# Kernel tuning notes

Hardware: AMD Instinct MI355X
Metric: run time of the kernel (lower is better)

Reference implementation:

```python
import jax, jax.numpy as jnp
import numpy as np

B, C, T = 32, 273, 4096
CHOUT = 270
N_SUBJECTS = 200
POS_DIM = 256
MARGIN = 0.2
INVALID = -0.1
N_FREQS = int((POS_DIM // 2) ** 0.5)          # 11
ACTUAL_POS_DIM = N_FREQS * N_FREQS * 2        # 242
NEG_INF = -1e9  # exp(-1e9)==0 in fp32, identical softmax to -inf but grad-safe


def fourier_emb(positions):
    # positions: [..., 2] -> [..., 2*n_freqs^2]
    freqs = jnp.arange(N_FREQS, dtype=positions.dtype)
    width = 1.0 + 2.0 * MARGIN
    p = positions + MARGIN
    scale = 2.0 * np.pi / width
    # loc[..., i, j] = x * f_i * scale + y * f_j * scale
    loc = (p[..., 0, None, None] * (scale * freqs[:, None])
           + p[..., 1, None, None] * (scale * freqs[None, :]))
    loc = loc.reshape(*positions.shape[:-1], N_FREQS * N_FREQS)
    return jnp.concatenate([jnp.cos(loc), jnp.sin(loc)], axis=-1)


def setup_inputs() -> dict:
    key = jax.random.key(0)
    k1, k2, k3, k4 = jax.random.split(key, 4)
    meg = jax.random.normal(k1, (B, C, T), dtype=jnp.float32)
    positions = jax.random.uniform(k2, (B, C, 2), dtype=jnp.float32)
    # last 16 channels per sample are invalid (sentinel -0.1 on both coords)
    positions = positions.at[:, -16:, :].set(INVALID)
    subject_index = jax.random.randint(k3, (B,), 0, N_SUBJECTS)
    heads = jax.random.normal(k4, (N_SUBJECTS, CHOUT, ACTUAL_POS_DIM),
                              dtype=jnp.float32) / np.sqrt(ACTUAL_POS_DIM)
    return {"meg": meg, "positions": positions,
            "subject_index": subject_index, "heads": heads}


def reference(meg, positions, subject_index, heads):
    # meg: [B,C,T], positions: [B,C,2], subject_index: [B],
    # heads: [n_subjects, chout, pos_dim]
    embedding = fourier_emb(positions)                       # [B,C,D]
    invalid = jnp.all(positions == INVALID, axis=-1)         # [B,C]
    score_offset = jnp.where(invalid, NEG_INF, 0.0).astype(meg.dtype)
    h = heads[subject_index]                                 # [B,chout,D] per-subject gather
    scores = jnp.einsum('bcd,bod->boc', embedding, h) + score_offset[:, None, :]
    weights = jax.nn.softmax(scores, axis=2)                 # softmax over channels
    out = jnp.einsum('bct,boc->bot', meg, weights)           # [B,chout,T]
    return out
```

## Files before the change

kernel.cpp:

```cpp
#include <hip/hip_runtime.h>

#define NB 32
#define NC 273
#define NT 4096
#define NO 270
#define ND 242
#define CK 288
#define TSUB 128
#define NSUB 4

typedef __attribute__((ext_vector_type(8))) short short8;
typedef __attribute__((ext_vector_type(4))) float f32x4;

__device__ __forceinline__ short f2bf(float f) {
    union { float f; unsigned int u; } x;
    x.f = f;
    unsigned int r = x.u + 0x7fffu + ((x.u >> 16) & 1u);
    return (short)(r >> 16);
}

__global__ void emb_kernel(const float* __restrict__ pos, float* __restrict__ emb) {
    const int g = blockIdx.x * 256 + threadIdx.x;
    const int TOT = NB * NC * 121;
    if (g >= TOT) return;
    const int p = g / 121;
    const int idx = g - p * 121;
    const int fi = idx / 11;
    const int fj = idx - fi * 11;
    const float scale = 4.487989505128276f;
    const float px = pos[p * 2] + 0.2f;
    const float py = pos[p * 2 + 1] + 0.2f;
    const float loc = px * (scale * (float)fi) + py * (scale * (float)fj);
    emb[(size_t)p * ND + idx] = cosf(loc);
    emb[(size_t)p * ND + 121 + idx] = sinf(loc);
}

__global__ __launch_bounds__(256) void scores_kernel(
    const float* __restrict__ emb, const float* __restrict__ heads,
    const int* __restrict__ subj, const float* __restrict__ pos,
    float* __restrict__ scores) {
    __shared__ float As[16 * 36];
    __shared__ float Bs[16 * 68];
    const int b = blockIdx.z;
    const int o0 = blockIdx.y * 32;
    const int c0 = blockIdx.x * 64;
    const int tid = threadIdx.x;
    const int s = subj[b];
    const int tx = tid & 15, ty = tid >> 4;
    const int srow = tid >> 3;
    const int sfp = tid & 7;

    float acc[2][4] = {};

    for (int kc = 0; kc < 256; kc += 16) {
        const int d = kc + sfp * 2;
        {
            const int o = o0 + srow;
            float2 av = make_float2(0.f, 0.f);
            if (d < ND && o < NO)
                av = *reinterpret_cast<const float2*>(
                    &heads[((size_t)(s * NO + o)) * ND + d]);
            As[(sfp * 2 + 0) * 36 + srow] = av.x;
            As[(sfp * 2 + 1) * 36 + srow] = av.y;
        }
#pragma unroll
        for (int half = 0; half < 2; ++half) {
            const int row = srow + half * 32;
            const int c = c0 + row;
            float2 bv = make_float2(0.f, 0.f);
            if (d < ND && c < NC)
                bv = *reinterpret_cast<const float2*>(
                    &emb[((size_t)(b * NC + c)) * ND + d]);
            Bs[(sfp * 2 + 0) * 68 + row] = bv.x;
            Bs[(sfp * 2 + 1) * 68 + row] = bv.y;
        }
        __syncthreads();
#pragma unroll
        for (int k = 0; k < 16; ++k) {
            const float2 a = *reinterpret_cast<const float2*>(&As[k * 36 + ty * 2]);
            const float4 bvv = *reinterpret_cast<const float4*>(&Bs[k * 68 + tx * 4]);
            const float aa[2] = {a.x, a.y};
            const float bb[4] = {bvv.x, bvv.y, bvv.z, bvv.w};
#pragma unroll
            for (int ii = 0; ii < 2; ++ii)
#pragma unroll
                for (int jj = 0; jj < 4; ++jj) acc[ii][jj] += aa[ii] * bb[jj];
        }
        __syncthreads();
    }

#pragma unroll
    for (int ii = 0; ii < 2; ++ii) {
        const int o = o0 + ty * 2 + ii;
        if (o >= NO) continue;
#pragma unroll
        for (int jj = 0; jj < 4; ++jj) {
            const int c = c0 + tx * 4 + jj;
            if (c >= NC) continue;
            const float px = pos[((size_t)(b * NC + c)) * 2];
            const float py = pos[((size_t)(b * NC + c)) * 2 + 1];
            const float off = (px == -0.1f && py == -0.1f) ? -1e9f : 0.0f;
            scores[((size_t)(b * NO + o)) * NC + c] = acc[ii][jj] + off;
        }
    }
}

__global__ __launch_bounds__(64) void softmax_kernel(float* __restrict__ scores) {
    const int row = blockIdx.x;
    float* s = scores + (size_t)row * NC;
    const int lane = threadIdx.x;

    float v[5];
    int cnt = 0;
    float mx = -1e30f;
    for (int c = lane; c < NC; c += 64) {
        v[cnt] = s[c];
        mx = fmaxf(mx, v[cnt]);
        ++cnt;
    }
#pragma unroll
    for (int off = 32; off; off >>= 1) mx = fmaxf(mx, __shfl_xor(mx, off));
    float sum = 0.0f;
    for (int i = 0; i < cnt; ++i) {
        v[i] = expf(v[i] - mx);
        sum += v[i];
    }
#pragma unroll
    for (int off = 32; off; off >>= 1) sum += __shfl_xor(sum, off);
    const float inv = 1.0f / sum;
    int i = 0;
    for (int c = lane; c < NC; c += 64) { s[c] = v[i++] * inv; }
}

__global__ __launch_bounds__(256) void transpose_kernel(
    const float* __restrict__ meg, short* __restrict__ megT) {
    __shared__ float lds[32 * 66];
    const int b = blockIdx.z;
    const int t0 = blockIdx.x * 32;
    const int c0 = blockIdx.y * 64;
    const int tx = threadIdx.x & 31;
    const int ty = threadIdx.x >> 5;
#pragma unroll
    for (int i = 0; i < 8; ++i) {
        const int cl = ty + i * 8;
        const int c = c0 + cl;
        float v = 0.f;
        if (c < NC) v = meg[((size_t)(b * NC + c)) * NT + t0 + tx];
        lds[tx * 66 + cl] = v;
    }
    __syncthreads();
    const int wx = threadIdx.x & 31;
    const int wy = threadIdx.x >> 5;
    const int c = c0 + wx * 2;
    if (c < CK) {
#pragma unroll
        for (int i = 0; i < 4; ++i) {
            const int tl = wy + i * 8;
            short2 v;
            v.x = f2bf(lds[tl * 66 + wx * 2]);
            v.y = f2bf(lds[tl * 66 + wx * 2 + 1]);
            *reinterpret_cast<short2*>(
                &megT[((size_t)(b * NT + t0 + tl)) * CK + c]) = v;
        }
    }
}

__global__ __launch_bounds__(256) void einsum_kernel(
    const short* __restrict__ megT, const float* __restrict__ wts,
    float* __restrict__ out) {
    __shared__ short Alds[9 * 4 * 64 * 8];
    const int b = blockIdx.z;
    const int o0 = blockIdx.y * 64;
    const int t0 = blockIdx.x * (TSUB * NSUB);
    const int tid = threadIdx.x;
    const int l = tid & 63;
    const int wv = tid >> 6;
    const int q = l >> 4;
    const int nlo = l & 15;

    {
        const int mt = wv;
        const int o = o0 + mt * 16 + nlo;
        const bool ov = (o < NO);
        const float* wrow = wts + ((size_t)(b * NO + (ov ? o : 0))) * NC;
        for (int ch = 0; ch < 9; ++ch) {
            const int k0 = ch * 32 + q * 8;
            short8 v;
#pragma unroll
            for (int j = 0; j < 8; ++j) {
                const int c = k0 + j;
                v[j] = f2bf((ov && c < NC) ? wrow[c] : 0.0f);
            }
            *reinterpret_cast<short8*>(&Alds[((ch * 4 + mt) * 64 + l) * 8]) = v;
        }
    }
    __syncthreads();

    f32x4 acc[4][2];
#pragma unroll
    for (int i = 0; i < 4; ++i)
#pragma unroll
        for (int j = 0; j < 2; ++j) acc[i][j] = {0.f, 0.f, 0.f, 0.f};

    const short* bbase = megT + ((size_t)(b * NT) + t0 + wv * 32 + nlo) * CK + q * 8;

    short8 Bq[3][2];
#pragma unroll
    for (int g = 0; g < 3; ++g) {
        Bq[g][0] = *reinterpret_cast<const short8*>(bbase + g * 32);
        Bq[g][1] = *reinterpret_cast<const short8*>(bbase + 16 * CK + g * 32);
    }

#pragma unroll
    for (int g = 0; g < 9 * NSUB; ++g) {
        const int st = g / 9;
        const int ch = g % 9;
        const int slot = g % 3;
#pragma unroll
        for (int mt = 0; mt < 4; ++mt) {
            const short8 av =
                *reinterpret_cast<const short8*>(&Alds[((ch * 4 + mt) * 64 + l) * 8]);
            acc[mt][0] = __builtin_amdgcn_mfma_f32_16x16x32_bf16(av, Bq[slot][0], acc[mt][0], 0, 0, 0);
            acc[mt][1] = __builtin_amdgcn_mfma_f32_16x16x32_bf16(av, Bq[slot][1], acc[mt][1], 0, 0, 0);
        }
        if (g + 3 < 9 * NSUB) {
            const int g2 = g + 3;
            const size_t off = (size_t)((g2 / 9) * TSUB) * CK + (g2 % 9) * 32;
            Bq[slot][0] = *reinterpret_cast<const short8*>(bbase + off);
            Bq[slot][1] = *reinterpret_cast<const short8*>(bbase + off + 16 * CK);
        }
        if (ch == 8) {
#pragma unroll
            for (int mt = 0; mt < 4; ++mt) {
                const int obase = o0 + mt * 16 + q * 4;
#pragma unroll
                for (int nf = 0; nf < 2; ++nf) {
                    const int t = t0 + st * TSUB + wv * 32 + nf * 16 + nlo;
#pragma unroll
                    for (int r = 0; r < 4; ++r) {
                        const int o = obase + r;
                        if (o < NO)
                            out[((size_t)(b * NO + o)) * NT + t] = acc[mt][nf][r];
                    }
                    acc[mt][nf] = {0.f, 0.f, 0.f, 0.f};
                }
            }
        }
    }
}

extern "C" void kernel_launch(void* const* d_in, const int* in_sizes, int n_in,
                              void* d_out, int out_size, void* d_ws, size_t ws_size,
                              hipStream_t stream) {
    const float* meg = (const float*)d_in[0];
    const float* pos = (const float*)d_in[1];
    const int* subj = (const int*)d_in[2];
    const float* heads = (const float*)d_in[3];
    float* out = (float*)d_out;

    float* emb = (float*)d_ws;
    float* scores = emb + (size_t)NB * NC * ND;
    short* megT = (short*)(scores + (size_t)NB * NO * NC);

    const int emb_items = NB * NC * 121;
    emb_kernel<<<dim3((emb_items + 255) / 256), dim3(256), 0, stream>>>(pos, emb);
    scores_kernel<<<dim3(5, 9, NB), dim3(256), 0, stream>>>(emb, heads, subj, pos, scores);
    softmax_kernel<<<dim3(NB * NO), dim3(64), 0, stream>>>(scores);
    transpose_kernel<<<dim3(NT / 32, 5, NB), dim3(256), 0, stream>>>(meg, megT);
    einsum_kernel<<<dim3(NT / (TSUB * NSUB), 5, NB), dim3(256), 0, stream>>>(megT, scores, out);
}
```

Measured before the change: 401.1 us.

## Fuse meg transpose into einsum and emit padded bf16 weights from softmax

Drops the separate transpose kernel that wrote a bf16 transposed copy of meg. The einsum kernel now reads fp32 meg directly with coalesced per-channel loads and converts to bf16 in registers. Softmax now writes zero-padded bf16 weights [B,288,288], so the einsum only stages bf16 tiles into LDS. Each einsum block now covers all output rows for a 64-wide time tile with 9x2 accumulators per wave, so meg is read once instead of being reread per output-row block. The trade-offs are more register pressure, two barriers per K chunk, and strided scalar global loads of meg.

New measurement: 376.9 us. -6.0%, faster.

```diff
diff --git a/kernel.cpp b/kernel.cpp
--- a/kernel.cpp
+++ b/kernel.cpp
@@ -5,9 +5,9 @@
 #define NT 4096
 #define NO 270
 #define ND 242
-#define CK 288
-#define TSUB 128
-#define NSUB 4
+#define OPAD 288
+#define CPAD 288
+#define TBLK 64
 
 typedef __attribute__((ext_vector_type(8))) short short8;
 typedef __attribute__((ext_vector_type(4))) float f32x4;
@@ -105,11 +105,20 @@
     }
 }
 
-__global__ __launch_bounds__(64) void softmax_kernel(float* __restrict__ scores) {
+__global__ __launch_bounds__(64) void softmax_kernel(
+    const float* __restrict__ scores, short* __restrict__ wbf) {
     const int row = blockIdx.x;
-    float* s = scores + (size_t)row * NC;
+    const int b = row / OPAD;
+    const int o = row - b * OPAD;
+    short* w = wbf + (size_t)row * CPAD;
     const int lane = threadIdx.x;
 
+    if (o >= NO) {
+        for (int c = lane; c < CPAD; c += 64) w[c] = 0;
+        return;
+    }
+
+    const float* s = scores + ((size_t)(b * NO + o)) * NC;
     float v[5];
     int cnt = 0;
     float mx = -1e30f;
@@ -129,121 +138,81 @@
     for (int off = 32; off; off >>= 1) sum += __shfl_xor(sum, off);
     const float inv = 1.0f / sum;
     int i = 0;
-    for (int c = lane; c < NC; c += 64) { s[c] = v[i++] * inv; }
-}
-
-__global__ __launch_bounds__(256) void transpose_kernel(
-    const float* __restrict__ meg, short* __restrict__ megT) {
-    __shared__ float lds[32 * 66];
+    for (int c = lane; c < CPAD; c += 64) {
+        float val = 0.0f;
+        if (c < NC) val = v[i++] * inv;
+        w[c] = f2bf(val);
+    }
+}
+
+__global__ __launch_bounds__(256) void einsum_kernel(
+    const float* __restrict__ meg, const short* __restrict__ wbf,
+    float* __restrict__ out) {
+    __shared__ short Alds[OPAD * 40];
     const int b = blockIdx.z;
-    const int t0 = blockIdx.x * 32;
-    const int c0 = blockIdx.y * 64;
-    const int tx = threadIdx.x & 31;
-    const int ty = threadIdx.x >> 5;
-#pragma unroll
-    for (int i = 0; i < 8; ++i) {
-        const int cl = ty + i * 8;
-        const int c = c0 + cl;
-        float v = 0.f;
-        if (c < NC) v = meg[((size_t)(b * NC + c)) * NT + t0 + tx];
-        lds[tx * 66 + cl] = v;
-    }
-    __syncthreads();
-    const int wx = threadIdx.x & 31;
-    const int wy = threadIdx.x >> 5;
-    const int c = c0 + wx * 2;
-    if (c < CK) {
-#pragma unroll
-        for (int i = 0; i < 4; ++i) {
-            const int tl = wy + i * 8;
-            short2 v;
-            v.x = f2bf(lds[tl * 66 + wx * 2]);
-            v.y = f2bf(lds[tl * 66 + wx * 2 + 1]);
-            *reinterpret_cast<short2*>(
-                &megT[((size_t)(b * NT + t0 + tl)) * CK + c]) = v;
-        }
-    }
-}
-
-__global__ __launch_bounds__(256) void einsum_kernel(
-    const short* __restrict__ megT, const float* __restrict__ wts,
-    float* __restrict__ out) {
-    __shared__ short Alds[9 * 4 * 64 * 8];
-    const int b = blockIdx.z;
-    const int o0 = blockIdx.y * 64;
-    const int t0 = blockIdx.x * (TSUB * NSUB);
+    const int t0 = blockIdx.x * TBLK;
     const int tid = threadIdx.x;
     const int l = tid & 63;
     const int wv = tid >> 6;
+    const int mw = wv >> 1;
+    const int tw = wv & 1;
     const int q = l >> 4;
     const int nlo = l & 15;
 
-    {
-        const int mt = wv;
-        const int o = o0 + mt * 16 + nlo;
-        const bool ov = (o < NO);
-        const float* wrow = wts + ((size_t)(b * NO + (ov ? o : 0))) * NC;
-        for (int ch = 0; ch < 9; ++ch) {
-            const int k0 = ch * 32 + q * 8;
-            short8 v;
-#pragma unroll
-            for (int j = 0; j < 8; ++j) {
-                const int c = k0 + j;
-                v[j] = f2bf((ov && c < NC) ? wrow[c] : 0.0f);
-            }
-            *reinterpret_cast<short8*>(&Alds[((ch * 4 + mt) * 64 + l) * 8]) = v;
-        }
-    }
-    __syncthreads();
-
-    f32x4 acc[4][2];
-#pragma unroll
-    for (int i = 0; i < 4; ++i)
+    f32x4 acc[9][2];
+#pragma unroll
+    for (int i = 0; i < 9; ++i)
 #pragma unroll
         for (int j = 0; j < 2; ++j) acc[i][j] = {0.f, 0.f, 0.f, 0.f};
 
-    const short* bbase = megT + ((size_t)(b * NT) + t0 + wv * 32 + nlo) * CK + q * 8;
-
-    short8 Bq[3][2];
-#pragma unroll
-    for (int g = 0; g < 3; ++g) {
-        Bq[g][0] = *reinterpret_cast<const short8*>(bbase + g * 32);
-        Bq[g][1] = *reinterpret_cast<const short8*>(bbase + 16 * CK + g * 32);
-    }
-
-#pragma unroll
-    for (int g = 0; g < 9 * NSUB; ++g) {
-        const int st = g / 9;
-        const int ch = g % 9;
-        const int slot = g % 3;
-#pragma unroll
-        for (int mt = 0; mt < 4; ++mt) {
-            const short8 av =
-                *reinterpret_cast<const short8*>(&Alds[((ch * 4 + mt) * 64 + l) * 8]);
-            acc[mt][0] = __builtin_amdgcn_mfma_f32_16x16x32_bf16(av, Bq[slot][0], acc[mt][0], 0, 0, 0);
-            acc[mt][1] = __builtin_amdgcn_mfma_f32_16x16x32_bf16(av, Bq[slot][1], acc[mt][1], 0, 0, 0);
-        }
-        if (g + 3 < 9 * NSUB) {
-            const int g2 = g + 3;
-            const size_t off = (size_t)((g2 / 9) * TSUB) * CK + (g2 % 9) * 32;
-            Bq[slot][0] = *reinterpret_cast<const short8*>(bbase + off);
-            Bq[slot][1] = *reinterpret_cast<const short8*>(bbase + off + 16 * CK);
-        }
-        if (ch == 8) {
-#pragma unroll
-            for (int mt = 0; mt < 4; ++mt) {
-                const int obase = o0 + mt * 16 + q * 4;
-#pragma unroll
-                for (int nf = 0; nf < 2; ++nf) {
-                    const int t = t0 + st * TSUB + wv * 32 + nf * 16 + nlo;
-#pragma unroll
-                    for (int r = 0; r < 4; ++r) {
-                        const int o = obase + r;
-                        if (o < NO)
-                            out[((size_t)(b * NO + o)) * NT + t] = acc[mt][nf][r];
-                    }
-                    acc[mt][nf] = {0.f, 0.f, 0.f, 0.f};
-                }
+    const float* mbase = meg + ((size_t)b * NC) * NT + t0 + tw * 32 + nlo;
+    const short* wbase = wbf + ((size_t)b * OPAD) * CPAD;
+
+    for (int kc = 0; kc < CPAD; kc += 32) {
+        float bf0[8], bf1[8];
+#pragma unroll
+        for (int j = 0; j < 8; ++j) {
+            int c = kc + q * 8 + j;
+            if (c >= NC) c = 0;
+            const float* mrow = mbase + (size_t)c * NT;
+            bf0[j] = mrow[0];
+            bf1[j] = mrow[16];
+        }
+        for (int sidx = tid; sidx < OPAD * 4; sidx += 256) {
+            const int row = sidx >> 2;
+            const int q4 = sidx & 3;
+            const short8 v = *reinterpret_cast<const short8*>(
+                wbase + (size_t)row * CPAD + kc + q4 * 8);
+            *reinterpret_cast<short8*>(&Alds[row * 40 + q4 * 8]) = v;
+        }
+        __syncthreads();
+        short8 b0, b1;
+#pragma unroll
+        for (int j = 0; j < 8; ++j) {
+            b0[j] = f2bf(bf0[j]);
+            b1[j] = f2bf(bf1[j]);
+        }
+#pragma unroll
+        for (int mt = 0; mt < 9; ++mt) {
+            const short8 av = *reinterpret_cast<const short8*>(
+                &Alds[(mw * 144 + mt * 16 + nlo) * 40 + q * 8]);
+            acc[mt][0] = __builtin_amdgcn_mfma_f32_16x16x32_bf16(av, b0, acc[mt][0], 0, 0, 0);
+            acc[mt][1] = __builtin_amdgcn_mfma_f32_16x16x32_bf16(av, b1, acc[mt][1], 0, 0, 0);
+        }
+        __syncthreads();
+    }
+
+    const int tcol = t0 + tw * 32 + nlo;
+#pragma unroll
+    for (int mt = 0; mt < 9; ++mt) {
+        const int ob = mw * 144 + mt * 16 + q * 4;
+#pragma unroll
+        for (int nf = 0; nf < 2; ++nf) {
+            const int t = tcol + nf * 16;
+#pragma unroll
+            for (int r = 0; r < 4; ++r) {
+                const int o = ob + r;
+                if (o < NO) out[((size_t)(b * NO + o)) * NT + t] = acc[mt][nf][r];
             }
         }
     }
@@ -260,12 +229,11 @@
 
     float* emb = (float*)d_ws;
     float* scores = emb + (size_t)NB * NC * ND;
-    short* megT = (short*)(scores + (size_t)NB * NO * NC);
+    short* wbf = (short*)(scores + (size_t)NB * NO * NC);
 
     const int emb_items = NB * NC * 121;
     emb_kernel<<<dim3((emb_items + 255) / 256), dim3(256), 0, stream>>>(pos, emb);
     scores_kernel<<<dim3(5, 9, NB), dim3(256), 0, stream>>>(emb, heads, subj, pos, scores);
-    softmax_kernel<<<dim3(NB * NO), dim3(64), 0, stream>>>(scores);
-    transpose_kernel<<<dim3(NT / 32, 5, NB), dim3(256), 0, stream>>>(meg, megT);
-    einsum_kernel<<<dim3(NT / (TSUB * NSUB), 5, NB), dim3(256), 0, stream>>>(megT, scores, out);
-}
+    softmax_kernel<<<dim3(NB * OPAD), dim3(64), 0, stream>>>(scores, wbf);
+    einsum_kernel<<<dim3(NT / TBLK, 1, NB), dim3(256), 0, stream>>>(meg, wbf, out);
+}
```
